# Kernel tuning notes

Hardware: AMD Instinct MI355X
Metric: run time of the kernel (lower is better)

Reference implementation:

```python
import jax, jax.numpy as jnp
import numpy as np
from jax import lax

T, B, E = 4096, 8, 512


def setup_inputs() -> dict:
    key = jax.random.key(0)
    k1, k2, k3 = jax.random.split(key, 3)
    x = jax.random.normal(k1, (T, B, E), dtype=jnp.float32)
    raw_pos_beta = jax.random.normal(k2, (E,), dtype=jnp.float32)
    raw_neg_beta = jax.random.normal(k3, (E,), dtype=jnp.float32)
    return {"x": x, "raw_pos_beta": raw_pos_beta, "raw_neg_beta": raw_neg_beta}


def reference(x, raw_pos_beta, raw_neg_beta):
    # pos/neg split EMA. The torch module computes out[t] = sum_{s<=t} beta^(t-s) u[s]
    # via a length-T depthwise conv; that is exactly the linear recurrence
    # mem[t] = beta * mem[t-1] + u[t], which we run as an O(T) scan.
    pos_beta = jax.nn.sigmoid(raw_pos_beta)  # [E]
    neg_beta = jax.nn.sigmoid(raw_neg_beta)  # [E]
    x_pos = jnp.where(x >= 0, x, 0.0) * (1.0 - pos_beta)  # [T,B,E]
    x_neg = jnp.where(x <= 0, x, 0.0) * (1.0 - neg_beta)  # [T,B,E]
    u = jnp.stack([x_pos, x_neg], axis=-1)                # [T,B,E,2]
    beta = jnp.stack([pos_beta, neg_beta], axis=-1)       # [E,2]

    def step(carry, u_t):
        new = beta * carry + u_t  # [B,E,2]
        return new, new

    init = jnp.zeros(u.shape[1:], dtype=x.dtype)
    _, mem2 = lax.scan(step, init, u)  # [T,B,E,2]
    return mem2[..., 0] + mem2[..., 1]  # [T,B,E]
```

## Files before the change

### kernel.cpp

```cpp
#include <hip/hip_runtime.h>


#define T_DIM 4096
#define B_DIM 8
#define E_DIM 512
#define CHUNK_L 16
#define NCHUNK (T_DIM / CHUNK_L)
#define BE (B_DIM * E_DIM)

__device__ __forceinline__ float sigmoidf_(float x) { return 1.0f / (1.0f + __expf(-x)); }

__global__ __launch_bounds__(256) void ParallelDLIEMA_17789754541002_kernel(
        const float* __restrict__ x,
        const float* __restrict__ rp,
        const float* __restrict__ rn,
        float* __restrict__ out) {
    int gtid = blockIdx.x * 256 + threadIdx.x;
    int e4 = gtid & 127;
    int b  = (gtid >> 7) & 7;
    int c  = gtid >> 10;
    int e  = e4 * 4;

    float4 rp4 = *(const float4*)(rp + e);
    float4 rn4 = *(const float4*)(rn + e);
    float bp[4] = {sigmoidf_(rp4.x), sigmoidf_(rp4.y), sigmoidf_(rp4.z), sigmoidf_(rp4.w)};
    float bn[4] = {sigmoidf_(rn4.x), sigmoidf_(rn4.y), sigmoidf_(rn4.z), sigmoidf_(rn4.w)};

    float fp4[4] = {0.f, 0.f, 0.f, 0.f};
    float fn4[4] = {0.f, 0.f, 0.f, 0.f};
    int base = c * CHUNK_L * BE + b * E_DIM + e;
    #pragma unroll
    for (int k = 0; k < CHUNK_L; k++) {
        float4 xv = *(const float4*)(x + base + k * BE);
        float f[4] = {xv.x, xv.y, xv.z, xv.w};
        #pragma unroll
        for (int j = 0; j < 4; j++) {
            fp4[j] = bp[j] * fp4[j] + fmaxf(f[j], 0.f) * (1.0f - bp[j]);
            fn4[j] = bn[j] * fn4[j] + fminf(f[j], 0.f) * (1.0f - bn[j]);
        }
    }
    *(float4*)(out + base + 0 * BE) = make_float4(fp4[0], fp4[1], fp4[2], fp4[3]);
    *(float4*)(out + base + 1 * BE) = make_float4(fn4[0], fn4[1], fn4[2], fn4[3]);
}

__global__ __launch_bounds__(256) void k_carry(const float* __restrict__ rp,
                                               const float* __restrict__ rn,
                                               float* __restrict__ out) {
    int gtid = blockIdx.x * 256 + threadIdx.x;
    int e = gtid & 511;
    int b = (gtid >> 9) & 7;
    int s = gtid >> 12;
    float beta = sigmoidf_(s ? rn[e] : rp[e]);
    float bl = beta * beta; bl = bl * bl; bl = bl * bl; bl = bl * bl;

    float* p = out + s * BE + b * E_DIM + e;
    float carry = 0.f;
    for (int g = 0; g < NCHUNK / 16; g++) {
        float fv[16];
        #pragma unroll
        for (int u = 0; u < 16; u++) fv[u] = p[(g * 16 + u) * (CHUNK_L * BE)];
        #pragma unroll
        for (int u = 0; u < 16; u++) {
            p[(g * 16 + u) * (CHUNK_L * BE)] = carry;
            carry = bl * carry + fv[u];
        }
    }
}

__global__ __launch_bounds__(256) void k_out(const float* __restrict__ x,
                                             const float* __restrict__ rp,
                                             const float* __restrict__ rn,
                                             float* __restrict__ out) {
    int gtid = blockIdx.x * 256 + threadIdx.x;
    int e4 = gtid & 127;
    int b  = (gtid >> 7) & 7;
    int c  = gtid >> 10;
    int e  = e4 * 4;

    float4 rp4 = *(const float4*)(rp + e);
    float4 rn4 = *(const float4*)(rn + e);
    float bp[4] = {sigmoidf_(rp4.x), sigmoidf_(rp4.y), sigmoidf_(rp4.z), sigmoidf_(rp4.w)};
    float bn[4] = {sigmoidf_(rn4.x), sigmoidf_(rn4.y), sigmoidf_(rn4.z), sigmoidf_(rn4.w)};

    int base = c * CHUNK_L * BE + b * E_DIM + e;
    float4 cp = *(const float4*)(out + base + 0 * BE);
    float4 cn = *(const float4*)(out + base + 1 * BE);
    float lp[4] = {cp.x, cp.y, cp.z, cp.w};
    float ln[4] = {cn.x, cn.y, cn.z, cn.w};

    #pragma unroll
    for (int k = 0; k < CHUNK_L; k++) {
        float4 xv = *(const float4*)(x + base + k * BE);
        float f[4] = {xv.x, xv.y, xv.z, xv.w};
        float o[4];
        #pragma unroll
        for (int j = 0; j < 4; j++) {
            lp[j] = bp[j] * lp[j] + fmaxf(f[j], 0.f) * (1.0f - bp[j]);
            ln[j] = bn[j] * ln[j] + fminf(f[j], 0.f) * (1.0f - bn[j]);
            o[j] = lp[j] + ln[j];
        }
        *(float4*)(out + base + k * BE) = make_float4(o[0], o[1], o[2], o[3]);
    }
}

extern "C" void kernel_launch(void* const* d_in, const int* in_sizes, int n_in,
                              void* d_out, int out_size, void* d_ws, size_t ws_size,
                              hipStream_t stream) {
    const float* x  = (const float*)d_in[0];
    const float* rp = (const float*)d_in[1];
    const float* rn = (const float*)d_in[2];
    float* out = (float*)d_out;

    ParallelDLIEMA_17789754541002_kernel<<<1024, 256, 0, stream>>>(x, rp, rn, out);
    k_carry<<<32, 256, 0, stream>>>(rp, rn, out);
    k_out<<<1024, 256, 0, stream>>>(x, rp, rn, out);
}
```

Before: 135.9 us.

## Fuse three-pass chunked scan into one cooperative kernel with grid syncs

Merges the chunk-local scan, the carry propagation and the output pass into a single cooperative kernel separated by two grid-wide syncs. Each thread keeps its 16 x float4 inputs in registers, so x is read from global memory once instead of twice, and two kernel launches go away. The carry phase now runs on only 32 of 1024 blocks while every other block waits at the grid barrier. The large register footprint and the cooperative residency requirement (1024 blocks co-resident, launch_bounds 256,4) risk a launch failure, in which case it falls back to the old three-kernel path.

```diff
diff --git a/kernel.cpp b/kernel.cpp
--- a/kernel.cpp
+++ b/kernel.cpp
@@ -1,4 +1,5 @@
 #include <hip/hip_runtime.h>
+#include <hip/hip_cooperative_groups.h>
 
 
 #define T_DIM 4096
@@ -8,9 +9,93 @@
 #define NCHUNK (T_DIM / CHUNK_L)
 #define BE (B_DIM * E_DIM)
 
+namespace cg = cooperative_groups;
+
 __device__ __forceinline__ float sigmoidf_(float x) { return 1.0f / (1.0f + __expf(-x)); }
 
-__global__ __launch_bounds__(256) void ParallelDLIEMA_17789754541002_kernel(
+__global__ __launch_bounds__(256, 4) void ParallelDLIEMA_17789754541002_kernel(
+        const float* __restrict__ x,
+        const float* __restrict__ rp,
+        const float* __restrict__ rn,
+        float* __restrict__ out) {
+    const int gtid = blockIdx.x * 256 + threadIdx.x;
+    const int e4 = gtid & 127;
+    const int b  = (gtid >> 7) & 7;
+    const int c  = gtid >> 10;
+    const int e  = e4 * 4;
+
+    float4 rp4 = *(const float4*)(rp + e);
+    float4 rn4 = *(const float4*)(rn + e);
+    float bp[4] = {sigmoidf_(rp4.x), sigmoidf_(rp4.y), sigmoidf_(rp4.z), sigmoidf_(rp4.w)};
+    float bn[4] = {sigmoidf_(rn4.x), sigmoidf_(rn4.y), sigmoidf_(rn4.z), sigmoidf_(rn4.w)};
+
+    const int base = c * CHUNK_L * BE + b * E_DIM + e;
+
+    float4 xr[CHUNK_L];
+    #pragma unroll
+    for (int k = 0; k < CHUNK_L; k++)
+        xr[k] = *(const float4*)(x + base + k * BE);
+
+    {
+        float fp[4] = {0.f, 0.f, 0.f, 0.f};
+        float fn[4] = {0.f, 0.f, 0.f, 0.f};
+        #pragma unroll
+        for (int k = 0; k < CHUNK_L; k++) {
+            float f[4] = {xr[k].x, xr[k].y, xr[k].z, xr[k].w};
+            #pragma unroll
+            for (int j = 0; j < 4; j++) {
+                fp[j] = bp[j] * fp[j] + fmaxf(f[j], 0.f) * (1.0f - bp[j]);
+                fn[j] = bn[j] * fn[j] + fminf(f[j], 0.f) * (1.0f - bn[j]);
+            }
+        }
+        *(float4*)(out + base)      = make_float4(fp[0], fp[1], fp[2], fp[3]);
+        *(float4*)(out + base + BE) = make_float4(fn[0], fn[1], fn[2], fn[3]);
+    }
+
+    cg::this_grid().sync();
+
+    if (gtid < 2 * BE) {
+        const int eb = gtid & 511;
+        const int bb = (gtid >> 9) & 7;
+        const int s  = gtid >> 12;
+        float beta = sigmoidf_(s ? rn[eb] : rp[eb]);
+        float bl = beta * beta; bl *= bl; bl *= bl; bl *= bl;
+        float* p = out + s * BE + bb * E_DIM + eb;
+        float carry = 0.f;
+        for (int g = 0; g < NCHUNK / 16; g++) {
+            float fv[16];
+            #pragma unroll
+            for (int u = 0; u < 16; u++) fv[u] = p[(g * 16 + u) * (CHUNK_L * BE)];
+            #pragma unroll
+            for (int u = 0; u < 16; u++) {
+                p[(g * 16 + u) * (CHUNK_L * BE)] = carry;
+                carry = bl * carry + fv[u];
+            }
+        }
+    }
+
+    cg::this_grid().sync();
+
+    float4 cp = *(const float4*)(out + base);
+    float4 cn = *(const float4*)(out + base + BE);
+    float lp[4] = {cp.x, cp.y, cp.z, cp.w};
+    float ln[4] = {cn.x, cn.y, cn.z, cn.w};
+    #pragma unroll
+    for (int k = 0; k < CHUNK_L; k++) {
+        float f[4] = {xr[k].x, xr[k].y, xr[k].z, xr[k].w};
+        float o[4];
+        #pragma unroll
+        for (int j = 0; j < 4; j++) {
+            lp[j] = bp[j] * lp[j] + fmaxf(f[j], 0.f) * (1.0f - bp[j]);
+            ln[j] = bn[j] * ln[j] + fminf(f[j], 0.f) * (1.0f - bn[j]);
+            o[j] = lp[j] + ln[j];
+        }
+        *(float4*)(out + base + k * BE) = make_float4(o[0], o[1], o[2], o[3]);
+    }
+}
+
+
+__global__ __launch_bounds__(256) void k1_local(
         const float* __restrict__ x,
         const float* __restrict__ rp,
         const float* __restrict__ rn,
@@ -111,7 +196,14 @@
     const float* rn = (const float*)d_in[2];
     float* out = (float*)d_out;
 
-    ParallelDLIEMA_17789754541002_kernel<<<1024, 256, 0, stream>>>(x, rp, rn, out);
-    k_carry<<<32, 256, 0, stream>>>(rp, rn, out);
-    k_out<<<1024, 256, 0, stream>>>(x, rp, rn, out);
-}
+    void* args[] = {(void*)&x, (void*)&rp, (void*)&rn, (void*)&out};
+    hipError_t err = hipLaunchCooperativeKernel(
+        (const void*)ParallelDLIEMA_17789754541002_kernel,
+        dim3(1024), dim3(256), args, 0, stream);
+
+    if (err != hipSuccess) {
+        k1_local<<<1024, 256, 0, stream>>>(x, rp, rn, out);
+        k_carry<<<32, 256, 0, stream>>>(rp, rn, out);
+        k_out<<<1024, 256, 0, stream>>>(x, rp, rn, out);
+    }
+}
```

Result: slower. 416.9 us (+206.7%).

## Parallelize chunk carry with wave-level scan and compact workspace for chunk finals

Applied to the files above, without the earlier changes.

The serial per-column carry pass over 256 chunks is replaced by a wavefront-parallel scan: each lane combines 4 chunk finals and a Hillis-Steele shuffle scan over 64 lanes propagates the carries, launched across 2048 blocks instead of 32. Chunk finals are stored in a compact workspace buffer when one is available, instead of strided slots inside the output, which improves locality for the carry pass. Output stores become nontemporal. The scan adds extra multiplies and depends on how much workspace is provided.

```diff
diff --git a/kernel.cpp b/kernel.cpp
--- a/kernel.cpp
+++ b/kernel.cpp
@@ -8,13 +8,15 @@
 #define NCHUNK (T_DIM / CHUNK_L)
 #define BE (B_DIM * E_DIM)
 
+typedef float f4_t __attribute__((ext_vector_type(4)));
+
 __device__ __forceinline__ float sigmoidf_(float x) { return 1.0f / (1.0f + __expf(-x)); }
 
 __global__ __launch_bounds__(256) void ParallelDLIEMA_17789754541002_kernel(
         const float* __restrict__ x,
         const float* __restrict__ rp,
         const float* __restrict__ rn,
-        float* __restrict__ out) {
+        float* __restrict__ fin, int cs) {
     int gtid = blockIdx.x * 256 + threadIdx.x;
     int e4 = gtid & 127;
     int b  = (gtid >> 7) & 7;
@@ -28,10 +30,10 @@
 
     float fp4[4] = {0.f, 0.f, 0.f, 0.f};
     float fn4[4] = {0.f, 0.f, 0.f, 0.f};
-    int base = c * CHUNK_L * BE + b * E_DIM + e;
+    int xbase = c * CHUNK_L * BE + b * E_DIM + e;
     #pragma unroll
     for (int k = 0; k < CHUNK_L; k++) {
-        float4 xv = *(const float4*)(x + base + k * BE);
+        float4 xv = *(const float4*)(x + xbase + k * BE);
         float f[4] = {xv.x, xv.y, xv.z, xv.w};
         #pragma unroll
         for (int j = 0; j < 4; j++) {
@@ -39,37 +41,52 @@
             fn4[j] = bn[j] * fn4[j] + fminf(f[j], 0.f) * (1.0f - bn[j]);
         }
     }
-    *(float4*)(out + base + 0 * BE) = make_float4(fp4[0], fp4[1], fp4[2], fp4[3]);
-    *(float4*)(out + base + 1 * BE) = make_float4(fn4[0], fn4[1], fn4[2], fn4[3]);
+    int fbase = c * cs + b * E_DIM + e;
+    *(float4*)(fin + fbase)      = make_float4(fp4[0], fp4[1], fp4[2], fp4[3]);
+    *(float4*)(fin + fbase + BE) = make_float4(fn4[0], fn4[1], fn4[2], fn4[3]);
 }
 
-__global__ __launch_bounds__(256) void k_carry(const float* __restrict__ rp,
-                                               const float* __restrict__ rn,
-                                               float* __restrict__ out) {
-    int gtid = blockIdx.x * 256 + threadIdx.x;
-    int e = gtid & 511;
-    int b = (gtid >> 9) & 7;
-    int s = gtid >> 12;
+__global__ __launch_bounds__(256) void k_carry_par(const float* __restrict__ rp,
+                                                   const float* __restrict__ rn,
+                                                   float* __restrict__ fin, int cs) {
+    int col  = blockIdx.x * 4 + (threadIdx.x >> 6);
+    int lane = threadIdx.x & 63;
+    int e = col & 511;
+    int b = (col >> 9) & 7;
+    int s = col >> 12;
     float beta = sigmoidf_(s ? rn[e] : rp[e]);
-    float bl = beta * beta; bl = bl * bl; bl = bl * bl; bl = bl * bl;
+    float bL = beta * beta; bL *= bL; bL *= bL; bL *= bL;
 
-    float* p = out + s * BE + b * E_DIM + e;
-    float carry = 0.f;
-    for (int g = 0; g < NCHUNK / 16; g++) {
-        float fv[16];
-        #pragma unroll
-        for (int u = 0; u < 16; u++) fv[u] = p[(g * 16 + u) * (CHUNK_L * BE)];
-        #pragma unroll
-        for (int u = 0; u < 16; u++) {
-            p[(g * 16 + u) * (CHUNK_L * BE)] = carry;
-            carry = bl * carry + fv[u];
-        }
+    float* p = fin + s * BE + b * E_DIM + e;
+    int c0 = lane * 4;
+    float f0 = p[(c0 + 0) * cs];
+    float f1 = p[(c0 + 1) * cs];
+    float f2 = p[(c0 + 2) * cs];
+    float f3 = p[(c0 + 3) * cs];
+
+    float B = ((f0 * bL + f1) * bL + f2) * bL + f3;
+    float bL2 = bL * bL;
+    float A = bL2 * bL2;
+
+    #pragma unroll
+    for (int d = 1; d < 64; d <<= 1) {
+        float Bu = __shfl_up(B, d);
+        float Au = __shfl_up(A, d);
+        if (lane >= d) { B = Bu * A + B; A = Au * A; }
     }
+    float prev = __shfl_up(B, 1);
+    float cin = (lane == 0) ? 0.f : prev;
+
+    p[(c0 + 0) * cs] = cin;  float t0 = bL * cin + f0;
+    p[(c0 + 1) * cs] = t0;   float t1 = bL * t0 + f1;
+    p[(c0 + 2) * cs] = t1;   float t2 = bL * t1 + f2;
+    p[(c0 + 3) * cs] = t2;
 }
 
 __global__ __launch_bounds__(256) void k_out(const float* __restrict__ x,
                                              const float* __restrict__ rp,
                                              const float* __restrict__ rn,
+                                             const float* __restrict__ fin, int cs,
                                              float* __restrict__ out) {
     int gtid = blockIdx.x * 256 + threadIdx.x;
     int e4 = gtid & 127;
@@ -82,12 +99,13 @@
     float bp[4] = {sigmoidf_(rp4.x), sigmoidf_(rp4.y), sigmoidf_(rp4.z), sigmoidf_(rp4.w)};
     float bn[4] = {sigmoidf_(rn4.x), sigmoidf_(rn4.y), sigmoidf_(rn4.z), sigmoidf_(rn4.w)};
 
-    int base = c * CHUNK_L * BE + b * E_DIM + e;
-    float4 cp = *(const float4*)(out + base + 0 * BE);
-    float4 cn = *(const float4*)(out + base + 1 * BE);
+    int fbase = c * cs + b * E_DIM + e;
+    float4 cp = *(const float4*)(fin + fbase);
+    float4 cn = *(const float4*)(fin + fbase + BE);
     float lp[4] = {cp.x, cp.y, cp.z, cp.w};
     float ln[4] = {cn.x, cn.y, cn.z, cn.w};
 
+    int base = c * CHUNK_L * BE + b * E_DIM + e;
     #pragma unroll
     for (int k = 0; k < CHUNK_L; k++) {
         float4 xv = *(const float4*)(x + base + k * BE);
@@ -99,7 +117,8 @@
             ln[j] = bn[j] * ln[j] + fminf(f[j], 0.f) * (1.0f - bn[j]);
             o[j] = lp[j] + ln[j];
         }
-        *(float4*)(out + base + k * BE) = make_float4(o[0], o[1], o[2], o[3]);
+        f4_t ov = {o[0], o[1], o[2], o[3]};
+        __builtin_nontemporal_store(ov, (f4_t*)(out + base + k * BE));
     }
 }
 
@@ -111,7 +130,18 @@
     const float* rn = (const float*)d_in[2];
     float* out = (float*)d_out;
 
-    ParallelDLIEMA_17789754541002_kernel<<<1024, 256, 0, stream>>>(x, rp, rn, out);
-    k_carry<<<32, 256, 0, stream>>>(rp, rn, out);
-    k_out<<<1024, 256, 0, stream>>>(x, rp, rn, out);
+    size_t need = (size_t)NCHUNK * 2 * BE * sizeof(float);
+    float* fin;
+    int cs;
+    if (ws_size >= need && d_ws != nullptr) {
+        fin = (float*)d_ws;
+        cs  = 2 * BE;
+    } else {
+        fin = out;
+        cs  = CHUNK_L * BE;
+    }
+
+    ParallelDLIEMA_17789754541002_kernel<<<1024, 256, 0, stream>>>(x, rp, rn, fin, cs);
+    k_carry_par<<<2048, 256, 0, stream>>>(rp, rn, fin, cs);
+    k_out<<<1024, 256, 0, stream>>>(x, rp, rn, fin, cs, out);
 }
```

After: 150.8 us. 1.11x slower.

## Fuse three-pass chunked scan into single kernel with decoupled cross-block flags

Applied to the files above, without the earlier changes.

Replaces the local-scan, carry and output kernels with one persistent-style kernel of 256 blocks of 1024 threads. Each block writes its chunk aggregate to workspace and raises a flag. The first 32 blocks sweep the carries in groups of 8 and publish done counters, and every block then spins on its predecessor group before emitting outputs. This removes two kernel launches and the extra round-trips through the output buffer, at the cost of spin-waiting. It assumes all blocks are co-resident (256 CUs on MI355X) to avoid deadlock, and it falls back to the old path when the workspace is too small.

```diff
diff --git a/kernel.cpp b/kernel.cpp
--- a/kernel.cpp
+++ b/kernel.cpp
@@ -7,27 +7,148 @@
 #define CHUNK_L 16
 #define NCHUNK (T_DIM / CHUNK_L)
 #define BE (B_DIM * E_DIM)
+#define NSWEEP 32
+#define GRP 8
+#define NGRP (NCHUNK / GRP)
 
 __device__ __forceinline__ float sigmoidf_(float x) { return 1.0f / (1.0f + __expf(-x)); }
 
-__global__ __launch_bounds__(256) void ParallelDLIEMA_17789754541002_kernel(
+__global__ __launch_bounds__(512) void k_zero_flags(unsigned int* __restrict__ flags) {
+    int i = threadIdx.x;
+    if (i < NCHUNK + NGRP) flags[i] = 0u;
+}
+
+__global__ __launch_bounds__(1024, 1) void ParallelDLIEMA_17789754541002_kernel(
         const float* __restrict__ x,
         const float* __restrict__ rp,
         const float* __restrict__ rn,
-        float* __restrict__ out) {
-    int gtid = blockIdx.x * 256 + threadIdx.x;
-    int e4 = gtid & 127;
-    int b  = (gtid >> 7) & 7;
-    int c  = gtid >> 10;
-    int e  = e4 * 4;
+        float* __restrict__ out,
+        float* __restrict__ ws) {
+    const int c   = blockIdx.x;
+    const int tid = threadIdx.x;
+    const int e   = (tid & 127) * 4;
+    const int b   = tid >> 7;
+    const int col = b * E_DIM + e;
+
+    float* agg  = ws;
+    float* incl = ws + 2 * NCHUNK * BE;
+    unsigned int* flag1 = (unsigned int*)(ws + 4 * NCHUNK * BE);
+    unsigned int* done2 = flag1 + NCHUNK;
 
     float4 rp4 = *(const float4*)(rp + e);
     float4 rn4 = *(const float4*)(rn + e);
     float bp[4] = {sigmoidf_(rp4.x), sigmoidf_(rp4.y), sigmoidf_(rp4.z), sigmoidf_(rp4.w)};
     float bn[4] = {sigmoidf_(rn4.x), sigmoidf_(rn4.y), sigmoidf_(rn4.z), sigmoidf_(rn4.w)};
 
-    float fp4[4] = {0.f, 0.f, 0.f, 0.f};
-    float fn4[4] = {0.f, 0.f, 0.f, 0.f};
+    const int xbase = c * CHUNK_L * BE + col;
+
+    float fp[4] = {0.f, 0.f, 0.f, 0.f};
+    float fn[4] = {0.f, 0.f, 0.f, 0.f};
+    #pragma unroll
+    for (int k = 0; k < CHUNK_L; k++) {
+        float4 xv = *(const float4*)(x + xbase + k * BE);
+        float f[4] = {xv.x, xv.y, xv.z, xv.w};
+        #pragma unroll
+        for (int j = 0; j < 4; j++) {
+            fp[j] = bp[j] * fp[j] + fmaxf(f[j], 0.f) * (1.0f - bp[j]);
+            fn[j] = bn[j] * fn[j] + fminf(f[j], 0.f) * (1.0f - bn[j]);
+        }
+    }
+
+    *(float4*)(agg + (size_t)(c * 2 + 0) * BE + col) = make_float4(fp[0], fp[1], fp[2], fp[3]);
+    *(float4*)(agg + (size_t)(c * 2 + 1) * BE + col) = make_float4(fn[0], fn[1], fn[2], fn[3]);
+    __syncthreads();
+    if (tid == 0) {
+        __threadfence();
+        __hip_atomic_store(&flag1[c], 1u, __ATOMIC_RELEASE, __HIP_MEMORY_SCOPE_AGENT);
+    }
+
+    if (c < NSWEEP && tid < 64) {
+        const int slot  = c * 64 + tid;
+        const int s     = slot >> 10;
+        const int q     = slot & 1023;
+        const int coff  = q * 4;
+        const int ebeta = (q & 127) * 4;
+
+        float4 rb = *(const float4*)((s ? rn : rp) + ebeta);
+        float bl[4] = {sigmoidf_(rb.x), sigmoidf_(rb.y), sigmoidf_(rb.z), sigmoidf_(rb.w)};
+        #pragma unroll
+        for (int j = 0; j < 4; j++) {
+            float t = bl[j] * bl[j]; t *= t; t *= t; t *= t; bl[j] = t;
+        }
+
+        float cr[4] = {0.f, 0.f, 0.f, 0.f};
+        for (int g = 0; g < NGRP; ++g) {
+            for (;;) {
+                unsigned f = __hip_atomic_load(&flag1[g * GRP + (tid & 7)],
+                                               __ATOMIC_RELAXED, __HIP_MEMORY_SCOPE_AGENT);
+                if (__all(f != 0u)) break;
+                __builtin_amdgcn_s_sleep(2);
+            }
+            __threadfence();
+            #pragma unroll
+            for (int u = 0; u < GRP; ++u) {
+                const int j = g * GRP + u;
+                const float4 a = *(const float4*)(agg + (size_t)(j * 2 + s) * BE + coff);
+                cr[0] = bl[0] * cr[0] + a.x;
+                cr[1] = bl[1] * cr[1] + a.y;
+                cr[2] = bl[2] * cr[2] + a.z;
+                cr[3] = bl[3] * cr[3] + a.w;
+                *(float4*)(incl + (size_t)(j * 2 + s) * BE + coff) =
+                    make_float4(cr[0], cr[1], cr[2], cr[3]);
+            }
+            __threadfence();
+            if (tid == 0)
+                __hip_atomic_fetch_add(&done2[g], 1u, __ATOMIC_RELEASE, __HIP_MEMORY_SCOPE_AGENT);
+        }
+    }
+
+    float lp[4] = {0.f, 0.f, 0.f, 0.f};
+    float ln[4] = {0.f, 0.f, 0.f, 0.f};
+    if (c > 0) {
+        const int g2 = (c - 1) >> 3;
+        const int lane = tid & 63;
+        unsigned v = 0;
+        for (;;) {
+            if (lane == 0)
+                v = __hip_atomic_load(&done2[g2], __ATOMIC_RELAXED, __HIP_MEMORY_SCOPE_AGENT);
+            v = __shfl(v, 0);
+            if (v >= (unsigned)NSWEEP) break;
+            __builtin_amdgcn_s_sleep(16);
+        }
+        __threadfence();
+        float4 cp = *(const float4*)(incl + (size_t)((c - 1) * 2 + 0) * BE + col);
+        float4 cn = *(const float4*)(incl + (size_t)((c - 1) * 2 + 1) * BE + col);
+        lp[0] = cp.x; lp[1] = cp.y; lp[2] = cp.z; lp[3] = cp.w;
+        ln[0] = cn.x; ln[1] = cn.y; ln[2] = cn.z; ln[3] = cn.w;
+    }
+
+    #pragma unroll
+    for (int k = 0; k < CHUNK_L; k++) {
+        float4 xv = *(const float4*)(x + xbase + k * BE);
+        float f[4] = {xv.x, xv.y, xv.z, xv.w};
+        float o[4];
+        #pragma unroll
+        for (int j = 0; j < 4; j++) {
+            lp[j] = bp[j] * lp[j] + fmaxf(f[j], 0.f) * (1.0f - bp[j]);
+            ln[j] = bn[j] * ln[j] + fminf(f[j], 0.f) * (1.0f - bn[j]);
+            o[j] = lp[j] + ln[j];
+        }
+        *(float4*)(out + xbase + k * BE) = make_float4(o[0], o[1], o[2], o[3]);
+    }
+}
+
+
+__global__ __launch_bounds__(256) void k1_local(
+        const float* __restrict__ x, const float* __restrict__ rp,
+        const float* __restrict__ rn, float* __restrict__ out) {
+    int gtid = blockIdx.x * 256 + threadIdx.x;
+    int e4 = gtid & 127; int b = (gtid >> 7) & 7; int c = gtid >> 10; int e = e4 * 4;
+    float4 rp4 = *(const float4*)(rp + e);
+    float4 rn4 = *(const float4*)(rn + e);
+    float bp[4] = {sigmoidf_(rp4.x), sigmoidf_(rp4.y), sigmoidf_(rp4.z), sigmoidf_(rp4.w)};
+    float bn[4] = {sigmoidf_(rn4.x), sigmoidf_(rn4.y), sigmoidf_(rn4.z), sigmoidf_(rn4.w)};
+    float fp4[4] = {0.f,0.f,0.f,0.f}, fn4[4] = {0.f,0.f,0.f,0.f};
     int base = c * CHUNK_L * BE + b * E_DIM + e;
     #pragma unroll
     for (int k = 0; k < CHUNK_L; k++) {
@@ -47,12 +168,9 @@
                                                const float* __restrict__ rn,
                                                float* __restrict__ out) {
     int gtid = blockIdx.x * 256 + threadIdx.x;
-    int e = gtid & 511;
-    int b = (gtid >> 9) & 7;
-    int s = gtid >> 12;
+    int e = gtid & 511; int b = (gtid >> 9) & 7; int s = gtid >> 12;
     float beta = sigmoidf_(s ? rn[e] : rp[e]);
     float bl = beta * beta; bl = bl * bl; bl = bl * bl; bl = bl * bl;
-
     float* p = out + s * BE + b * E_DIM + e;
     float carry = 0.f;
     for (int g = 0; g < NCHUNK / 16; g++) {
@@ -72,22 +190,16 @@
                                              const float* __restrict__ rn,
                                              float* __restrict__ out) {
     int gtid = blockIdx.x * 256 + threadIdx.x;
-    int e4 = gtid & 127;
-    int b  = (gtid >> 7) & 7;
-    int c  = gtid >> 10;
-    int e  = e4 * 4;
-
+    int e4 = gtid & 127; int b = (gtid >> 7) & 7; int c = gtid >> 10; int e = e4 * 4;
     float4 rp4 = *(const float4*)(rp + e);
     float4 rn4 = *(const float4*)(rn + e);
     float bp[4] = {sigmoidf_(rp4.x), sigmoidf_(rp4.y), sigmoidf_(rp4.z), sigmoidf_(rp4.w)};
     float bn[4] = {sigmoidf_(rn4.x), sigmoidf_(rn4.y), sigmoidf_(rn4.z), sigmoidf_(rn4.w)};
-
     int base = c * CHUNK_L * BE + b * E_DIM + e;
     float4 cp = *(const float4*)(out + base + 0 * BE);
     float4 cn = *(const float4*)(out + base + 1 * BE);
     float lp[4] = {cp.x, cp.y, cp.z, cp.w};
     float ln[4] = {cn.x, cn.y, cn.z, cn.w};
-
     #pragma unroll
     for (int k = 0; k < CHUNK_L; k++) {
         float4 xv = *(const float4*)(x + base + k * BE);
@@ -111,7 +223,16 @@
     const float* rn = (const float*)d_in[2];
     float* out = (float*)d_out;
 
-    ParallelDLIEMA_17789754541002_kernel<<<1024, 256, 0, stream>>>(x, rp, rn, out);
-    k_carry<<<32, 256, 0, stream>>>(rp, rn, out);
-    k_out<<<1024, 256, 0, stream>>>(x, rp, rn, out);
-}
+    const size_t need = (size_t)4 * NCHUNK * BE * sizeof(float)
+                        + (NCHUNK + NGRP) * sizeof(unsigned int);
+    if (d_ws != nullptr && ws_size >= need) {
+        float* ws = (float*)d_ws;
+        unsigned int* flags = (unsigned int*)(ws + 4 * NCHUNK * BE);
+        k_zero_flags<<<1, 512, 0, stream>>>(flags);
+        ParallelDLIEMA_17789754541002_kernel<<<NCHUNK, 1024, 0, stream>>>(x, rp, rn, out, ws);
+    } else {
+        k1_local<<<1024, 256, 0, stream>>>(x, rp, rn, out);
+        k_carry<<<32, 256, 0, stream>>>(rp, rn, out);
+        k_out<<<1024, 256, 0, stream>>>(x, rp, rn, out);
+    }
+}
```

Result: slower. 517.4 us (+280.6%).
